# Optimization experiments

Measured on AMD Instinct MI355X. Metric: run time of the kernel, lower is better.

Reference implementation:

```python
import jax, jax.numpy as jnp
import numpy as np

# Static diagonal offsets of the SparseDIA matrix (eqx static field).
OFFSETS = (-128, -64, -8, -1, 0, 1, 8, 64, 128)
N = 8192   # matrix dimension (diags.shape[1])
M = 4096   # number of dense columns in `other`


def setup_inputs() -> dict:
    key = jax.random.key(0)
    k1, k2 = jax.random.split(key)
    diags = jax.random.normal(k1, (len(OFFSETS), N), dtype=jnp.float32)
    other = jax.random.normal(k2, (N, M), dtype=jnp.float32)
    return {"diags": diags, "other": other}


def reference(diags, other):
    """SparseDIA._matmul_dense(left_matmul=True): out = A_dia @ other.

    For each static offset k, rows [top:bottom] of the output accumulate
    diag[start:end] (the valid part of the stored diagonal) times the
    matching rows of `other`. Offsets are Python ints, so all slices are
    static and jit-compatible.
    """
    n = other.shape[0]
    out = jnp.zeros_like(other)
    for k, offset in enumerate(OFFSETS):
        start = max(0, offset)
        end = min(n, n + offset)
        top = max(0, -offset)
        bottom = top + (end - start)
        out = out.at[top:bottom, :].add(
            diags[k, start:end, None] * other[start:end, :]
        )
    return out
```

## Files before the change

kernel.cpp:

```cpp
#include <hip/hip_runtime.h>


#define DIA_N 8192
#define DIA_M 4096
#define M4 (DIA_M / 4)
#define TR 16

typedef float f4 __attribute__((ext_vector_type(4)));

__global__ __launch_bounds__(256, 4) void sparse_dia_kernel(
    const float* __restrict__ diags,
    const float* __restrict__ other,
    float* __restrict__ out)
{
    const int r0 = blockIdx.y * TR;
    const int c4 = blockIdx.x * 256 + threadIdx.x;

    const f4* __restrict__ o4 = (const f4*)other;
    f4* __restrict__ out4     = (f4*)out;

    f4 acc[TR];
#pragma unroll
    for (int i = 0; i < TR; ++i) acc[i] = (f4){0.f, 0.f, 0.f, 0.f};

    if (r0 >= 128 && r0 + TR + 128 <= DIA_N) {

        constexpr int FOFF[4] = {-128, -64, 64, 128};
        constexpr int FK[4]   = {0, 1, 7, 8};
#pragma unroll
        for (int f = 0; f < 4; ++f) {
            const int off = FOFF[f];
            const int k   = FK[f];
#pragma unroll
            for (int i = 0; i < TR; ++i) {
                const int q   = r0 + i + off;
                const float d = diags[k * DIA_N + q];
                const f4 v    = o4[q * M4 + c4];
                acc[i] += d * v;
            }
        }

#pragma unroll
        for (int j = -8; j < TR + 8; ++j) {
            const int q = r0 + j;
            const f4 v  = o4[q * M4 + c4];
            if (j + 8 >= 0 && j + 8 < TR) acc[j + 8] += diags[2 * DIA_N + q] * v;
            if (j + 1 >= 0 && j + 1 < TR) acc[j + 1] += diags[3 * DIA_N + q] * v;
            if (j     >= 0 && j     < TR) acc[j    ] += diags[4 * DIA_N + q] * v;
            if (j - 1 >= 0 && j - 1 < TR) acc[j - 1] += diags[5 * DIA_N + q] * v;
            if (j - 8 >= 0 && j - 8 < TR) acc[j - 8] += diags[6 * DIA_N + q] * v;
        }
    } else {
        constexpr int OFF[9] = {-128, -64, -8, -1, 0, 1, 8, 64, 128};
#pragma unroll
        for (int k = 0; k < 9; ++k) {
#pragma unroll
            for (int i = 0; i < TR; ++i) {
                const int q = r0 + i + OFF[k];
                if (q >= 0 && q < DIA_N) {
                    const float d = diags[k * DIA_N + q];
                    const f4 v    = o4[q * M4 + c4];
                    acc[i] += d * v;
                }
            }
        }
    }

#pragma unroll
    for (int i = 0; i < TR; ++i) {
        __builtin_nontemporal_store(acc[i], &out4[(r0 + i) * M4 + c4]);
    }
}

extern "C" void kernel_launch(void* const* d_in, const int* in_sizes, int n_in,
                              void* d_out, int out_size, void* d_ws, size_t ws_size,
                              hipStream_t stream) {
    const float* diags = (const float*)d_in[0];
    const float* other = (const float*)d_in[1];
    float* out         = (float*)d_out;

    dim3 block(256, 1, 1);
    dim3 grid(M4 / 256, DIA_N / TR, 1);
    sparse_dia_kernel<<<grid, block, 0, stream>>>(diags, other, out);
}
```

Baseline: 285.2 us.

## Remap blocks to XCD-aware column slabs with 64-row bands per block

Each block now handles a 64-row band as four wavefronts of 16 rows each over a 64-wide column slice, with block IDs decoded so that all blocks on one XCD (bid & 7) share a 128-float4 column range. The goal is to keep the stencil's overlapping row halos in each XCD's own L2, cutting redundant HBM reads of `other`. The change also replaces nontemporal stores with normal stores and drops the occupancy hint from launch_bounds. Risks are narrower per-row coalescing (256 bytes per wave) and store traffic now polluting the cache.

```diff
diff --git a/kernel.cpp b/kernel.cpp
--- a/kernel.cpp
+++ b/kernel.cpp
@@ -3,73 +3,73 @@
 
 #define DIA_N 8192
 #define DIA_M 4096
-#define M4 (DIA_M / 4)
-#define TR 16
+#define M4    (DIA_M / 4)
+#define TRR   16
 
 typedef float f4 __attribute__((ext_vector_type(4)));
 
-__global__ __launch_bounds__(256, 4) void sparse_dia_kernel(
+__global__ __launch_bounds__(256) void sparse_dia_kernel(
     const float* __restrict__ diags,
     const float* __restrict__ other,
     float* __restrict__ out)
 {
-    const int r0 = blockIdx.y * TR;
-    const int c4 = blockIdx.x * 256 + threadIdx.x;
+    const int bid  = blockIdx.x;
+    const int xcd  = bid & 7;
+    const int w    = bid >> 3;
+    const int sub  = w >> 7;
+    const int band = w & 127;
+    const int lane = threadIdx.x & 63;
+    const int slot = threadIdx.x >> 6;
 
-    const f4* __restrict__ o4 = (const f4*)other;
-    f4* __restrict__ out4     = (f4*)out;
+    const int r0 = band * 64 + slot * TRR;
+    const int c4 = xcd * 128 + sub * 64 + lane;
 
-    f4 acc[TR];
+    const f4* __restrict__ o4   = (const f4*)other;
+    f4* __restrict__       out4 = (f4*)out;
+
+    f4 acc[TRR];
 #pragma unroll
-    for (int i = 0; i < TR; ++i) acc[i] = (f4){0.f, 0.f, 0.f, 0.f};
+    for (int i = 0; i < TRR; ++i) acc[i] = (f4){0.f, 0.f, 0.f, 0.f};
 
-    if (r0 >= 128 && r0 + TR + 128 <= DIA_N) {
+    if (band >= 2 && band <= 125) {
 
         constexpr int FOFF[4] = {-128, -64, 64, 128};
         constexpr int FK[4]   = {0, 1, 7, 8};
 #pragma unroll
         for (int f = 0; f < 4; ++f) {
-            const int off = FOFF[f];
-            const int k   = FK[f];
 #pragma unroll
-            for (int i = 0; i < TR; ++i) {
-                const int q   = r0 + i + off;
-                const float d = diags[k * DIA_N + q];
-                const f4 v    = o4[q * M4 + c4];
-                acc[i] += d * v;
+            for (int i = 0; i < TRR; ++i) {
+                const int q = r0 + i + FOFF[f];
+                acc[i] += diags[FK[f] * DIA_N + q] * o4[(size_t)q * M4 + c4];
             }
         }
 
 #pragma unroll
-        for (int j = -8; j < TR + 8; ++j) {
+        for (int j = -8; j < TRR + 8; ++j) {
             const int q = r0 + j;
-            const f4 v  = o4[q * M4 + c4];
-            if (j + 8 >= 0 && j + 8 < TR) acc[j + 8] += diags[2 * DIA_N + q] * v;
-            if (j + 1 >= 0 && j + 1 < TR) acc[j + 1] += diags[3 * DIA_N + q] * v;
-            if (j     >= 0 && j     < TR) acc[j    ] += diags[4 * DIA_N + q] * v;
-            if (j - 1 >= 0 && j - 1 < TR) acc[j - 1] += diags[5 * DIA_N + q] * v;
-            if (j - 8 >= 0 && j - 8 < TR) acc[j - 8] += diags[6 * DIA_N + q] * v;
+            const f4 v  = o4[(size_t)q * M4 + c4];
+            if (j + 8 >= 0 && j + 8 < TRR) acc[j + 8] += diags[2 * DIA_N + q] * v;
+            if (j + 1 >= 0 && j + 1 < TRR) acc[j + 1] += diags[3 * DIA_N + q] * v;
+            if (j     >= 0 && j     < TRR) acc[j    ] += diags[4 * DIA_N + q] * v;
+            if (j - 1 >= 0 && j - 1 < TRR) acc[j - 1] += diags[5 * DIA_N + q] * v;
+            if (j - 8 >= 0 && j - 8 < TRR) acc[j - 8] += diags[6 * DIA_N + q] * v;
         }
     } else {
         constexpr int OFF[9] = {-128, -64, -8, -1, 0, 1, 8, 64, 128};
 #pragma unroll
         for (int k = 0; k < 9; ++k) {
 #pragma unroll
-            for (int i = 0; i < TR; ++i) {
+            for (int i = 0; i < TRR; ++i) {
                 const int q = r0 + i + OFF[k];
-                if (q >= 0 && q < DIA_N) {
-                    const float d = diags[k * DIA_N + q];
-                    const f4 v    = o4[q * M4 + c4];
-                    acc[i] += d * v;
-                }
+                if (q >= 0 && q < DIA_N)
+                    acc[i] += diags[k * DIA_N + q] * o4[(size_t)q * M4 + c4];
             }
         }
     }
 
 #pragma unroll
-    for (int i = 0; i < TR; ++i) {
-        __builtin_nontemporal_store(acc[i], &out4[(r0 + i) * M4 + c4]);
-    }
+    for (int i = 0; i < TRR; ++i)
+        out4[(size_t)(r0 + i) * M4 + c4] = acc[i];
 }
 
 extern "C" void kernel_launch(void* const* d_in, const int* in_sizes, int n_in,
@@ -80,6 +80,6 @@
     float* out         = (float*)d_out;
 
     dim3 block(256, 1, 1);
-    dim3 grid(M4 / 256, DIA_N / TR, 1);
+    dim3 grid(2048, 1, 1);
     sparse_dia_kernel<<<grid, block, 0, stream>>>(diags, other, out);
 }
```

Measured after the change: 276.4 us. 1.03x faster.
